# Kernel optimization log

Measured on AMD Instinct MI355X. Metric: run time of the kernel, lower is better.

Reference implementation:

```python
import jax, jax.numpy as jnp
import numpy as np

V = 32000   # vocab_size
D = 64      # rnn_size == input_size (hard-coded in InstEncoder)
B = 16384   # batch
T = 64      # instruction length


def setup_inputs() -> dict:
    key = jax.random.key(0)
    ks = jax.random.split(key, 24)
    s = 0.05
    inp = {}
    # tokens in [1, V] so every position is non-zero -> last hidden is the final LSTM state
    inp['inst'] = jax.random.randint(ks[0], (B, T), 1, V + 1, dtype=jnp.int32)
    # canvas cells: [color, shape, row, col], small non-negative ints, stored as float
    inp['canvas'] = jax.random.randint(ks[1], (B, 25, 4), 0, 5).astype(jnp.float32)
    # 1 = absolute instruction, 2 = relative instruction
    inp['inst_type'] = jax.random.randint(ks[2], (B,), 1, 3, dtype=jnp.int32)
    # parameters
    inp['embed'] = jax.random.normal(ks[3], (V + 1, D)) * s
    inp['W_ih'] = jax.random.normal(ks[4], (D, 4 * D)) * s
    inp['W_hh'] = jax.random.normal(ks[5], (D, 4 * D)) * s
    inp['b_ih'] = jnp.zeros((4 * D,))
    inp['b_hh'] = jnp.zeros((4 * D,))
    inp['Wc'] = jax.random.normal(ks[6], (D, 3)) * s;  inp['bc'] = jnp.zeros((3,))
    inp['Ws'] = jax.random.normal(ks[7], (D, 3)) * s;  inp['bs'] = jnp.zeros((3,))
    inp['Wa'] = jax.random.normal(ks[8], (D, 2)) * s;  inp['ba'] = jnp.zeros((2,))
    inp['Wl'] = jax.random.normal(ks[9], (D, 25)) * s; inp['bl'] = jnp.zeros((25,))
    inp['Wr'] = jax.random.normal(ks[10], (D, 8)) * s; inp['br'] = jnp.zeros((8,))
    inp['Wr1'] = jax.random.normal(ks[11], (D + 4, 32)) * s; inp['br1'] = jnp.zeros((32,))
    inp['Wr2'] = jax.random.normal(ks[12], (32, 1)) * s;     inp['br2'] = jnp.zeros((1,))
    return inp


def _lstm_last_hidden(tokens, embed, W_ih, W_hh, b_ih, b_hh):
    x = embed[tokens]                      # [B, T, D]
    n = x.shape[0]
    h0 = jnp.zeros((n, D), x.dtype)
    c0 = jnp.zeros((n, D), x.dtype)

    def step(carry, xt):
        h, c = carry
        gates = xt @ W_ih + h @ W_hh + (b_ih + b_hh)   # [B, 4D], torch gate order i,f,g,o
        i, f, g, o = jnp.split(gates, 4, axis=-1)
        c = jax.nn.sigmoid(f) * c + jax.nn.sigmoid(i) * jnp.tanh(g)
        h = jax.nn.sigmoid(o) * jnp.tanh(c)
        return (h, c), None

    (h, _), _ = jax.lax.scan(step, (h0, c0), jnp.swapaxes(x, 0, 1))
    return h                               # [B, D]


def _sample_head(logits, k):
    logp = jax.nn.log_softmax(logits, axis=-1)
    samp = jax.random.categorical(k, logits, axis=-1)
    lp = jnp.take_along_axis(logp, samp[:, None], axis=-1)[:, 0]
    return samp, lp


def reference(inst, canvas, inst_type, embed, W_ih, W_hh, b_ih, b_hh,
              Wc, bc, Ws, bs, Wa, ba, Wl, bl, Wr, br, Wr1, br1, Wr2, br2):
    n = inst.shape[0]
    e = _lstm_last_hidden(inst, embed, W_ih, W_hh, b_ih, b_hh)   # [B, 64]

    key = jax.random.key(42)
    k_color, k_shape, k_act, k_abs, k_rel, k_att = jax.random.split(key, 6)

    color_s, color_lp = _sample_head(e @ Wc + bc, k_color)   # 3-way
    shape_s, shape_lp = _sample_head(e @ Ws + bs, k_shape)   # 3-way
    act_s,   act_lp   = _sample_head(e @ Wa + ba, k_act)     # 2-way (pred_act=True)

    # absolute location head: 25-way
    abs_loc_s, abs_loc_lp = _sample_head(e @ Wl + bl, k_abs)

    # relative: 8-way offset head + ref-object attention over 25 canvas cells
    rel_s, rel_lp = _sample_head(e @ Wr + br, k_rel)
    att_in = jnp.concatenate(
        [jnp.broadcast_to(e[:, None, :], (n, 25, D)), canvas], axis=-1)   # [B, 25, 68]
    att_logits = (jax.nn.relu(att_in @ Wr1 + br1) @ Wr2 + br2)[..., 0]    # [B, 25]
    att_s, att_lp = _sample_head(att_logits, k_att)
    # gather the attended canvas cell (vectorized version of the per-row .cpu() loop)
    ref_obj = jnp.take_along_axis(canvas, att_s[:, None, None], axis=1)[:, 0, :].astype(jnp.int32)

    offsets = jnp.array([[-1, 0], [1, 0], [0, 1], [0, -1],
                         [-1, -1], [-1, 1], [1, -1], [1, 1]], dtype=jnp.int32)
    off = offsets[rel_s]                                                  # [B, 2]
    rel_loc = (ref_obj[:, 2] + off[:, 0]) * 5 + (ref_obj[:, 3] + off[:, 1])

    # vectorized index_join: ref_type 0 -> abs path, 1 -> rel path
    is_rel = (inst_type - 1) == 1
    loc_predict = jnp.where(is_rel, rel_loc, abs_loc_s.astype(jnp.int32))
    loc_lp = jnp.where(is_rel, rel_lp, abs_loc_lp)
    att_lp = jnp.where(is_rel, att_lp, jnp.zeros_like(att_lp))

    log_probs = jnp.stack([color_lp, shape_lp, act_lp, loc_lp, att_lp], axis=-1)  # [B, 5]
    return log_probs, loc_predict
```

## Files before the change

### kernel.cpp

```cpp
#include <hip/hip_runtime.h>
#include <hip/hip_bf16.h>
#include <stdint.h>


__device__ __forceinline__ uint32_t rotl32(uint32_t x, uint32_t r) {
  return (x << r) | (x >> (32u - r));
}

__device__ __forceinline__ uint2 threefry2x32(uint32_t k0, uint32_t k1,
                                              uint32_t x0, uint32_t x1) {
  const uint32_t k2 = k0 ^ k1 ^ 0x1BD11BDAu;
  x0 += k0; x1 += k1;
#define TFR(r) { x0 += x1; x1 = rotl32(x1, r); x1 ^= x0; }
  TFR(13u) TFR(15u) TFR(26u) TFR(6u)
  x0 += k1; x1 += k2 + 1u;
  TFR(17u) TFR(29u) TFR(16u) TFR(24u)
  x0 += k2; x1 += k0 + 2u;
  TFR(13u) TFR(15u) TFR(26u) TFR(6u)
  x0 += k0; x1 += k1 + 3u;
  TFR(17u) TFR(29u) TFR(16u) TFR(24u)
  x0 += k1; x1 += k2 + 4u;
  TFR(13u) TFR(15u) TFR(26u) TFR(6u)
  x0 += k2; x1 += k0 + 5u;
#undef TFR
  return make_uint2(x0, x1);
}

__device__ __forceinline__ float gumbel_jax(uint32_t k0, uint32_t k1, uint32_t idx) {
  uint2 o = threefry2x32(k0, k1, 0u, idx);
  uint32_t bits = o.x ^ o.y;
  float f = __uint_as_float(0x3f800000u | (bits >> 9)) - 1.0f;
  const float tiny = 1.1754943508222875e-38f;
  float u = fmaxf(tiny, f + tiny);
  return -logf(-logf(u));
}

template <int C>
__device__ __forceinline__ void sample_head(const float* lg, uint32_t k0, uint32_t k1,
                                            int row, int& samp, float& lp) {
  float best = -3.402823466e38f;
  int bi = 0;
  float lsel = lg[0];
  float m = lg[0];
  #pragma unroll
  for (int c = 0; c < C; ++c) {
    float t = lg[c] + gumbel_jax(k0, k1, (uint32_t)(row * C + c));
    if (t > best) { best = t; bi = c; lsel = lg[c]; }
    m = fmaxf(m, lg[c]);
  }
  float s = 0.f;
  #pragma unroll
  for (int c = 0; c < C; ++c) s += expf(lg[c] - m);
  samp = bi;
  lp = lsel - m - logf(s);
}

__device__ __forceinline__ float sigmoidf_(float x) { return 1.0f / (1.0f + expf(-x)); }

__global__ __launch_bounds__(1024) void k_embedw(
    const float* __restrict__ embed, const float* __restrict__ W_ih,
    const float* __restrict__ b_ih, const float* __restrict__ b_hh,
    float* __restrict__ embedWG, int NV) {
  __shared__ float sW[64 * 256];
  const int tid = threadIdx.x;
  for (int i = tid; i < 4096; i += 1024)
    ((float4*)sW)[i] = ((const float4*)W_ih)[i];
  __syncthreads();
  const int d   = tid & 63;
  const int gi  = (tid >> 6) & 3;
  const int vr0 = tid >> 8;
  const int g   = gi * 64 + d;
  const float bias = b_ih[g] + b_hh[g];
  const int vbase = blockIdx.x * 126;
  for (int it = 0; it < 32; ++it) {
    int lr = it * 4 + vr0;
    int v  = vbase + lr;
    if (lr < 126 && v < NV) {
      const float* e = embed + (size_t)v * 64;
      float acc = bias;
      #pragma unroll 8
      for (int k = 0; k < 64; ++k) acc = fmaf(e[k], sW[k * 256 + g], acc);
      embedWG[(size_t)v * 256 + d * 4 + gi] = acc;
    }
  }
}

__global__ __launch_bounds__(1024) void k_lstm64(
    const int* __restrict__ inst, const float* __restrict__ W_hh,
    const float* __restrict__ embedWG, float* __restrict__ eOut) {
  extern __shared__ float smem[];
  float* sW = smem;
  float* sH = smem + 16384;

  const int tid = threadIdx.x;
  const int l   = tid & 63;
  const int wid = tid >> 6;
  const int d0  = wid << 2;
  const int rbase = blockIdx.x << 6;
  const size_t r  = (size_t)rbase + l;

  for (int i = tid; i < 16384; i += 1024) {
    int k = i >> 8, g = i & 255;
    sW[(g & 63) * 256 + k * 4 + (g >> 6)] = W_hh[i];
  }
  for (int i = tid; i < 4096; i += 1024) sH[i] = 0.f;
  __syncthreads();

  float c[4] = {0.f, 0.f, 0.f, 0.f};
  float4 gc[4], gn[4];
  int tok1;
  {
    int tok0 = inst[r * 64 + 0];
    tok1     = inst[r * 64 + 1];
    const float4* p = (const float4*)(embedWG + (size_t)tok0 * 256 + d0 * 4);
    #pragma unroll
    for (int i = 0; i < 4; ++i) gc[i] = p[i];
  }

  const float4* wv = (const float4*)sW;

  for (int t = 0; t < 64; ++t) {
    {
      const float4* p = (const float4*)(embedWG + (size_t)tok1 * 256 + d0 * 4);
      #pragma unroll
      for (int i = 0; i < 4; ++i) gn[i] = p[i];
    }
    int tok2 = inst[r * 64 + (t + 2 < 64 ? t + 2 : 63)];

    float a[4][4];
    #pragma unroll
    for (int u = 0; u < 4; ++u) {
      a[u][0] = gc[u].x; a[u][1] = gc[u].y; a[u][2] = gc[u].z; a[u][3] = gc[u].w;
    }

    #pragma unroll 4
    for (int k = 0; k < 64; ++k) {
      float hk = sH[k * 64 + l];
      #pragma unroll
      for (int u = 0; u < 4; ++u) {
        float4 w = wv[(d0 + u) * 64 + k];
        a[u][0] = fmaf(hk, w.x, a[u][0]);
        a[u][1] = fmaf(hk, w.y, a[u][1]);
        a[u][2] = fmaf(hk, w.z, a[u][2]);
        a[u][3] = fmaf(hk, w.w, a[u][3]);
      }
    }
    __syncthreads();
    #pragma unroll
    for (int u = 0; u < 4; ++u) {
      float ig = sigmoidf_(a[u][0]);
      float fg = sigmoidf_(a[u][1]);
      float gg = tanhf(a[u][2]);
      float og = sigmoidf_(a[u][3]);
      float cn = fg * c[u] + ig * gg;
      c[u] = cn;
      sH[(d0 + u) * 64 + l] = og * tanhf(cn);
    }
    __syncthreads();
    #pragma unroll
    for (int i = 0; i < 4; ++i) gc[i] = gn[i];
    tok1 = tok2;
  }

  for (int i = tid; i < 4096; i += 1024) {
    int rr = i >> 6, dd = i & 63;
    eOut[(size_t)(rbase + rr) * 64 + dd] = sH[dd * 64 + rr];
  }
}

__global__ __launch_bounds__(256) void k_attlog(
    const float* __restrict__ eOut, const float* __restrict__ canvas,
    const float* __restrict__ Wr1, const float* __restrict__ br1,
    const float* __restrict__ Wr2, const float* __restrict__ br2,
    float* __restrict__ attL, int total) {
  const int gid = blockIdx.x * 256 + threadIdx.x;
  if (gid >= total) return;
  const int rrow = gid / 25, cell = gid - rrow * 25;
  const float* e  = eOut + (size_t)rrow * 64;
  const float* cv = canvas + (size_t)rrow * 100 + cell * 4;
  float cv0 = cv[0], cv1 = cv[1], cv2 = cv[2], cv3 = cv[3];

  float h[32];
  #pragma unroll
  for (int j4 = 0; j4 < 8; ++j4) {
    float4 b4 = ((const float4*)br1)[j4];
    float4 w64 = ((const float4*)(Wr1 + 64 * 32))[j4];
    float4 w65 = ((const float4*)(Wr1 + 65 * 32))[j4];
    float4 w66 = ((const float4*)(Wr1 + 66 * 32))[j4];
    float4 w67 = ((const float4*)(Wr1 + 67 * 32))[j4];
    h[j4*4+0] = fmaf(cv3, w67.x, fmaf(cv2, w66.x, fmaf(cv1, w65.x, fmaf(cv0, w64.x, b4.x))));
    h[j4*4+1] = fmaf(cv3, w67.y, fmaf(cv2, w66.y, fmaf(cv1, w65.y, fmaf(cv0, w64.y, b4.y))));
    h[j4*4+2] = fmaf(cv3, w67.z, fmaf(cv2, w66.z, fmaf(cv1, w65.z, fmaf(cv0, w64.z, b4.z))));
    h[j4*4+3] = fmaf(cv3, w67.w, fmaf(cv2, w66.w, fmaf(cv1, w65.w, fmaf(cv0, w64.w, b4.w))));
  }
  for (int k = 0; k < 64; ++k) {
    float ek = e[k];
    const float4* wrow = (const float4*)(Wr1 + k * 32);
    #pragma unroll
    for (int j4 = 0; j4 < 8; ++j4) {
      float4 w = wrow[j4];
      h[j4*4+0] = fmaf(ek, w.x, h[j4*4+0]);
      h[j4*4+1] = fmaf(ek, w.y, h[j4*4+1]);
      h[j4*4+2] = fmaf(ek, w.z, h[j4*4+2]);
      h[j4*4+3] = fmaf(ek, w.w, h[j4*4+3]);
    }
  }
  float logit = br2[0];
  #pragma unroll
  for (int j = 0; j < 32; ++j) logit = fmaf(fmaxf(h[j], 0.f), Wr2[j], logit);
  attL[gid] = logit;
}

__global__ __launch_bounds__(256) void k_heads(
    const float* __restrict__ eOut, const float* __restrict__ canvas,
    const int* __restrict__ inst_type,
    const float* __restrict__ Wc, const float* __restrict__ bc,
    const float* __restrict__ Wsh, const float* __restrict__ bsh,
    const float* __restrict__ Wa, const float* __restrict__ ba,
    const float* __restrict__ Wl, const float* __restrict__ bl,
    const float* __restrict__ Wr, const float* __restrict__ br,
    const float* __restrict__ attL, float* __restrict__ out, int B) {
  const int r = blockIdx.x * 256 + threadIdx.x;
  if (r >= B) return;
  const float* e = eOut + (size_t)r * 64;

  uint2 kc  = threefry2x32(0u, 42u, 0u, 0u);
  uint2 ksh = threefry2x32(0u, 42u, 0u, 1u);
  uint2 kac = threefry2x32(0u, 42u, 0u, 2u);
  uint2 kab = threefry2x32(0u, 42u, 0u, 3u);
  uint2 krl = threefry2x32(0u, 42u, 0u, 4u);
  uint2 kat = threefry2x32(0u, 42u, 0u, 5u);

  float lc[3]  = {bc[0], bc[1], bc[2]};
  float lsh[3] = {bsh[0], bsh[1], bsh[2]};
  float lac[2] = {ba[0], ba[1]};
  float ll[25];
  #pragma unroll
  for (int j = 0; j < 25; ++j) ll[j] = bl[j];
  float lrr[8];
  #pragma unroll
  for (int j = 0; j < 8; ++j) lrr[j] = br[j];

  for (int k = 0; k < 64; ++k) {
    float ek = e[k];
    #pragma unroll
    for (int j = 0; j < 3; ++j)  lc[j]  = fmaf(ek, Wc[k * 3 + j],  lc[j]);
    #pragma unroll
    for (int j = 0; j < 3; ++j)  lsh[j] = fmaf(ek, Wsh[k * 3 + j], lsh[j]);
    #pragma unroll
    for (int j = 0; j < 2; ++j)  lac[j] = fmaf(ek, Wa[k * 2 + j],  lac[j]);
    #pragma unroll
    for (int j = 0; j < 25; ++j) ll[j]  = fmaf(ek, Wl[k * 25 + j], ll[j]);
    #pragma unroll
    for (int j = 0; j < 8; ++j)  lrr[j] = fmaf(ek, Wr[k * 8 + j],  lrr[j]);
  }

  int s_color, s_shape, s_act, s_abs, s_rel, s_att;
  float lp_color, lp_shape, lp_act, lp_abs, lp_rel, lp_att;
  sample_head<3>(lc,  kc.x,  kc.y,  r, s_color, lp_color);
  sample_head<3>(lsh, ksh.x, ksh.y, r, s_shape, lp_shape);
  sample_head<2>(lac, kac.x, kac.y, r, s_act,   lp_act);
  sample_head<25>(ll, kab.x, kab.y, r, s_abs,   lp_abs);
  sample_head<8>(lrr, krl.x, krl.y, r, s_rel,   lp_rel);

  float lat[25];
  #pragma unroll
  for (int j = 0; j < 25; ++j) lat[j] = attL[(size_t)r * 25 + j];
  sample_head<25>(lat, kat.x, kat.y, r, s_att, lp_att);

  const float* cvp = canvas + (size_t)r * 100 + s_att * 4;
  int ref_r = (int)cvp[2];
  int ref_c = (int)cvp[3];
  int dr = (int)((0x22001120u >> (4 * s_rel)) & 15u) - 1;
  int dc = (int)((0x20200211u >> (4 * s_rel)) & 15u) - 1;
  int rel_loc = (ref_r + dr) * 5 + (ref_c + dc);

  bool isrel = (inst_type[r] == 2);
  out[(size_t)r * 5 + 0] = lp_color;
  out[(size_t)r * 5 + 1] = lp_shape;
  out[(size_t)r * 5 + 2] = lp_act;
  out[(size_t)r * 5 + 3] = isrel ? lp_rel : lp_abs;
  out[(size_t)r * 5 + 4] = isrel ? lp_att : 0.f;
  out[(size_t)B * 5 + r] = (float)(isrel ? rel_loc : s_abs);
}

extern "C" void kernel_launch(void* const* d_in, const int* in_sizes, int n_in,
                              void* d_out, int out_size, void* d_ws, size_t ws_size,
                              hipStream_t stream) {
  (void)n_in; (void)out_size; (void)ws_size;
  const int*   inst      = (const int*)  d_in[0];
  const float* canvas    = (const float*)d_in[1];
  const int*   inst_type = (const int*)  d_in[2];
  const float* embed     = (const float*)d_in[3];
  const float* W_ih      = (const float*)d_in[4];
  const float* W_hh      = (const float*)d_in[5];
  const float* b_ih      = (const float*)d_in[6];
  const float* b_hh      = (const float*)d_in[7];
  const float* Wc  = (const float*)d_in[8];  const float* bc  = (const float*)d_in[9];
  const float* Wsh = (const float*)d_in[10]; const float* bsh = (const float*)d_in[11];
  const float* Wa  = (const float*)d_in[12]; const float* ba  = (const float*)d_in[13];
  const float* Wl  = (const float*)d_in[14]; const float* bl  = (const float*)d_in[15];
  const float* Wr  = (const float*)d_in[16]; const float* br  = (const float*)d_in[17];
  const float* Wr1 = (const float*)d_in[18]; const float* br1 = (const float*)d_in[19];
  const float* Wr2 = (const float*)d_in[20]; const float* br2 = (const float*)d_in[21];

  const int B  = in_sizes[0] / 64;
  const int NV = in_sizes[3] / 64;

  float* embedWG = (float*)d_ws;
  float* eOut    = embedWG + (size_t)NV * 256;
  float* attL    = eOut + (size_t)B * 64;
  float* out     = (float*)d_out;

  hipFuncSetAttribute((const void*)k_lstm64,
                      hipFuncAttributeMaxDynamicSharedMemorySize, 81920);

  k_embedw<<<(NV + 125) / 126, 1024, 0, stream>>>(embed, W_ih, b_ih, b_hh, embedWG, NV);
  k_lstm64<<<B / 64, 1024, 81920, stream>>>(inst, W_hh, embedWG, eOut);
  {
    int total = B * 25;
    k_attlog<<<(total + 255) / 256, 256, 0, stream>>>(eOut, canvas, Wr1, br1, Wr2, br2,
                                                      attL, total);
  }
  k_heads<<<(B + 255) / 256, 256, 0, stream>>>(eOut, canvas, inst_type,
                                               Wc, bc, Wsh, bsh, Wa, ba, Wl, bl, Wr, br,
                                               attL, out, B);
}
```

Before: 1.009 ms.

## Read W_hh via wave-uniform scalar loads instead of shared memory in LSTM kernel

```diff
diff --git a/kernel.cpp b/kernel.cpp
--- a/kernel.cpp
+++ b/kernel.cpp
@@ -85,12 +85,20 @@
   }
 }
 
+__global__ __launch_bounds__(1024) void k_wt(const float* __restrict__ W_hh,
+                                             float* __restrict__ wt) {
+  const int idx = blockIdx.x * 1024 + threadIdx.x;
+  if (idx < 16384) {
+    const int k = idx >> 8, g = idx & 255;
+    const int gi = g >> 6, u = g & 63;
+    wt[k * 256 + u * 4 + gi] = W_hh[idx];
+  }
+}
+
 __global__ __launch_bounds__(1024) void k_lstm64(
-    const int* __restrict__ inst, const float* __restrict__ W_hh,
+    const int* __restrict__ inst, const float* __restrict__ wt,
     const float* __restrict__ embedWG, float* __restrict__ eOut) {
-  extern __shared__ float smem[];
-  float* sW = smem;
-  float* sH = smem + 16384;
+  __shared__ float sH[4096];
 
   const int tid = threadIdx.x;
   const int l   = tid & 63;
@@ -99,10 +107,8 @@
   const int rbase = blockIdx.x << 6;
   const size_t r  = (size_t)rbase + l;
 
-  for (int i = tid; i < 16384; i += 1024) {
-    int k = i >> 8, g = i & 255;
-    sW[(g & 63) * 256 + k * 4 + (g >> 6)] = W_hh[i];
-  }
+  const float* __restrict__ wp = wt + __builtin_amdgcn_readfirstlane(wid * 16);
+
   for (int i = tid; i < 4096; i += 1024) sH[i] = 0.f;
   __syncthreads();
 
@@ -117,8 +123,6 @@
     for (int i = 0; i < 4; ++i) gc[i] = p[i];
   }
 
-  const float4* wv = (const float4*)sW;
-
   for (int t = 0; t < 64; ++t) {
     {
       const float4* p = (const float4*)(embedWG + (size_t)tok1 * 256 + d0 * 4);
@@ -136,14 +140,10 @@
     #pragma unroll 4
     for (int k = 0; k < 64; ++k) {
       float hk = sH[k * 64 + l];
+      const float* __restrict__ wk = wp + k * 256;
       #pragma unroll
-      for (int u = 0; u < 4; ++u) {
-        float4 w = wv[(d0 + u) * 64 + k];
-        a[u][0] = fmaf(hk, w.x, a[u][0]);
-        a[u][1] = fmaf(hk, w.y, a[u][1]);
-        a[u][2] = fmaf(hk, w.z, a[u][2]);
-        a[u][3] = fmaf(hk, w.w, a[u][3]);
-      }
+      for (int j = 0; j < 16; ++j)
+        a[j >> 2][j & 3] = fmaf(hk, wk[j], a[j >> 2][j & 3]);
     }
     __syncthreads();
     #pragma unroll
@@ -310,13 +310,12 @@
   float* embedWG = (float*)d_ws;
   float* eOut    = embedWG + (size_t)NV * 256;
   float* attL    = eOut + (size_t)B * 64;
+  float* wtbuf   = attL + (size_t)B * 25;
   float* out     = (float*)d_out;
 
-  hipFuncSetAttribute((const void*)k_lstm64,
-                      hipFuncAttributeMaxDynamicSharedMemorySize, 81920);
-
   k_embedw<<<(NV + 125) / 126, 1024, 0, stream>>>(embed, W_ih, b_ih, b_hh, embedWG, NV);
-  k_lstm64<<<B / 64, 1024, 81920, stream>>>(inst, W_hh, embedWG, eOut);
+  k_wt<<<16, 1024, 0, stream>>>(W_hh, wtbuf);
+  k_lstm64<<<B / 64, 1024, 0, stream>>>(inst, wtbuf, embedWG, eOut);
   {
     int total = B * 25;
     k_attlog<<<(total + 255) / 256, 256, 0, stream>>>(eOut, canvas, Wr1, br1, Wr2, br2,
```

New measurement: 841.5 us. 16.6% less time.
